# Kernel optimization log

Hardware: AMD Instinct MI355X
Metric: run time of the kernel (lower is better)

Reference implementation:

```python
import jax, jax.numpy as jnp
import numpy as np

D_MODEL = 128; D_STATE = 64; HEADDIM = 64; CHUNK = 64; EXPAND = 2
D_INNER = EXPAND * D_MODEL            # 256
NHEADS = D_INNER // HEADDIM           # 4
NGROUPS = 1; D_CONV = 4
D_XBC = D_INNER + 2 * NGROUPS * D_STATE          # 384
D_IN_PROJ = 2 * D_INNER + 2 * NGROUPS * D_STATE + NHEADS  # 644


def _segsum(x):
    # x: (..., L) -> (..., L, L) with [i, j] = sum_{j<k<=i} x_k, -inf above diag
    L = x.shape[-1]
    cs = jnp.cumsum(x, -1)
    d = cs[..., :, None] - cs[..., None, :]
    mask = jnp.tril(jnp.ones((L, L), bool))
    return jnp.where(mask, d, -jnp.inf)


def _mamba2(x, Wi, conv_w, conv_b, dt_bias, A_log, Dp, norm_w, Wo):
    b, l, _ = x.shape
    zxbcdt = x @ Wi.T                                    # (b,l,644)
    z = zxbcdt[..., :D_INNER]
    xBC = zxbcdt[..., D_INNER:D_INNER + D_XBC]
    dt = jax.nn.softplus(zxbcdt[..., D_INNER + D_XBC:] + dt_bias)  # (b,l,h)
    # causal depthwise conv1d, kernel 4
    xp = jnp.pad(xBC, ((0, 0), (D_CONV - 1, 0), (0, 0)))
    xBC = sum(xp[:, k:k + l, :] * conv_w[:, k] for k in range(D_CONV)) + conv_b
    xBC = jax.nn.silu(xBC)
    xs = xBC[..., :D_INNER].reshape(b, l, NHEADS, HEADDIM)
    Bm = xBC[..., D_INNER:D_INNER + D_STATE]             # (b,l,n) ngroups=1
    Cm = xBC[..., D_INNER + D_STATE:]                    # (b,l,n)
    A = -jnp.exp(A_log)                                  # (h,)
    # chunked SSD (ssd_minimal style)
    c = l // CHUNK
    X = xs.reshape(b, c, CHUNK, NHEADS, HEADDIM)
    dtc = dt.reshape(b, c, CHUNK, NHEADS)
    Bc = Bm.reshape(b, c, CHUNK, D_STATE)
    Cc = Cm.reshape(b, c, CHUNK, D_STATE)
    dA = jnp.transpose(dtc * A, (0, 3, 1, 2))            # (b,h,c,L)
    Acs = jnp.cumsum(dA, -1)
    Lm = jnp.exp(_segsum(dA))                            # (b,h,c,L,L)
    Xdt = X * dtc[..., None]                             # (b,c,L,h,p)
    Yd = jnp.einsum('bcln,bcsn,bhcls,bcshp->bclhp', Cc, Bc, Lm, Xdt)
    dec = jnp.exp(Acs[..., -1:] - Acs)                   # (b,h,c,L)
    st = jnp.einsum('bcln,bhcl,bclhp->bchpn', Bc, dec, Xdt)  # per-chunk states
    cd = jnp.exp(Acs[..., -1])                           # (b,h,c)
    def step(carry, inp):
        s, d = inp                                       # s:(b,h,p,n), d:(b,h)
        return carry * d[..., None, None] + s, carry
    init = jnp.zeros_like(st[:, 0])
    _, prev = jax.lax.scan(step, init, (jnp.moveaxis(st, 1, 0), jnp.moveaxis(cd, 2, 0)))
    prev = jnp.moveaxis(prev, 0, 1)                      # (b,c,h,p,n)
    Yo = jnp.einsum('bcln,bchpn,bhcl->bclhp', Cc, prev, jnp.exp(Acs))
    Y = (Yd + Yo).reshape(b, l, NHEADS, HEADDIM) + Dp[None, None, :, None] * xs
    # gated RMSNorm (norm_before_gate=False)
    y = Y.reshape(b, l, D_INNER) * jax.nn.silu(z)
    y = y * jax.lax.rsqrt(jnp.mean(y * y, -1, keepdims=True) + 1e-5) * norm_w
    return y @ Wo.T


def _init_params(key):
    ks = jax.random.split(key, 5)
    dt = jnp.exp(jax.random.uniform(ks[2], (NHEADS,)) * (np.log(0.1) - np.log(0.001)) + np.log(0.001))
    return {
        'Wi': jax.random.normal(ks[0], (D_IN_PROJ, D_MODEL), jnp.float32) * (D_MODEL ** -0.5),
        'conv_w': jax.random.normal(ks[1], (D_XBC, D_CONV), jnp.float32) * 0.3,
        'conv_b': jnp.zeros((D_XBC,), jnp.float32),
        'dt_bias': jnp.log(jnp.expm1(dt)),
        'A_log': jnp.log(jax.random.uniform(ks[3], (NHEADS,)) * 15.0 + 1.0),
        'D': jnp.ones((NHEADS,), jnp.float32),
        'norm_w': jnp.ones((D_INNER,), jnp.float32),
        'Wo': jax.random.normal(ks[4], (D_MODEL, D_INNER), jnp.float32) * (D_INNER ** -0.5),
    }


def setup_inputs() -> dict:
    key = jax.random.key(0)
    kx, kf, kb = jax.random.split(key, 3)
    inp = {'x': jax.random.normal(kx, (16, 2048, D_MODEL), jnp.float32)}
    for sfx, kk in (('_f', kf), ('_b', kb)):
        p = _init_params(kk)
        for name, v in p.items():
            inp[name + sfx] = v
    return inp


def reference(x, Wi_f, conv_w_f, conv_b_f, dt_bias_f, A_log_f, D_f, norm_w_f, Wo_f,
              Wi_b, conv_w_b, conv_b_b, dt_bias_b, A_log_b, D_b, norm_w_b, Wo_b):
    h_f = _mamba2(x, Wi_f, conv_w_f, conv_b_f, dt_bias_f, A_log_f, D_f, norm_w_f, Wo_f)
    h_b = jnp.flip(_mamba2(jnp.flip(x, 1), Wi_b, conv_w_b, conv_b_b, dt_bias_b, A_log_b, D_b, norm_w_b, Wo_b), 1)
    return h_f + h_b
```

## Files before the change

kernel.cpp:

```cpp
#include <hip/hip_runtime.h>
#include <hip/hip_bf16.h>
#include <cmath>

#define B_    16
#define L_    2048
#define T_    32768
#define DM_   128
#define DI_   256
#define DXBC_ 384
#define DS_   64
#define HD_   64
#define NH_   4
#define NC_   32

typedef __hip_bfloat16 bf16;
typedef __attribute__((ext_vector_type(8))) short short8;
typedef __attribute__((ext_vector_type(4))) float f32x4;

__device__ __forceinline__ float b2f(bf16 v) { return __bfloat162float(v); }
__device__ __forceinline__ bf16  f2b(float f) { return __float2bfloat16(f); }
__device__ __forceinline__ short f2bs(float f) { bf16 h = __float2bfloat16(f); return *reinterpret_cast<short*>(&h); }
__device__ __forceinline__ float bs2f(short s) { bf16 h = *reinterpret_cast<bf16*>(&s); return __bfloat162float(h); }
__device__ __forceinline__ float frcp_(float x) { return __builtin_amdgcn_rcpf(x); }
__device__ __forceinline__ float sigmoidf_(float x) { return frcp_(1.f + __expf(-x)); }
__device__ __forceinline__ float softplusf_(float x) { return (x > 20.f) ? x : __logf(1.f + __expf(x)); }
__device__ __forceinline__ float expneg_(float x) { return __expf(fminf(x, 0.f)); }

struct __align__(8) S4 { short a, b, c, d; };

#define NWI 82432
#define NWO 32768

__global__ __launch_bounds__(256) void k_prep(
    const float* __restrict__ x,
    const float* __restrict__ WiF, const float* __restrict__ WiB,
    const float* __restrict__ WoF, const float* __restrict__ WoB,
    bf16* __restrict__ Xb, bf16* __restrict__ WiFb, bf16* __restrict__ WiBb,
    bf16* __restrict__ WoFb, bf16* __restrict__ WoBb)
{
    const int gid = blockIdx.x * 256 + threadIdx.x;
    const int stride = gridDim.x * 256;
    for (int i = gid; i < 1048576; i += stride) {
        float4 v = ((const float4*)x)[i];
        S4 s = { f2bs(v.x), f2bs(v.y), f2bs(v.z), f2bs(v.w) };
        ((S4*)Xb)[i] = s;
    }
    for (int i = gid; i < NWI / 4; i += stride) {
        float4 v = ((const float4*)WiF)[i];
        S4 s = { f2bs(v.x), f2bs(v.y), f2bs(v.z), f2bs(v.w) };
        ((S4*)WiFb)[i] = s;
        v = ((const float4*)WiB)[i];
        S4 t = { f2bs(v.x), f2bs(v.y), f2bs(v.z), f2bs(v.w) };
        ((S4*)WiBb)[i] = t;
    }
    for (int i = gid; i < NWO / 4; i += stride) {
        float4 v = ((const float4*)WoF)[i];
        S4 s = { f2bs(v.x), f2bs(v.y), f2bs(v.z), f2bs(v.w) };
        ((S4*)WoFb)[i] = s;
        v = ((const float4*)WoB)[i];
        S4 t = { f2bs(v.x), f2bs(v.y), f2bs(v.z), f2bs(v.w) };
        ((S4*)WoBb)[i] = t;
    }
}

__global__ __launch_bounds__(256) void k_inproj_mfma(
    const bf16* __restrict__ Xb, const bf16* __restrict__ WiFb, const bf16* __restrict__ WiBb,
    const float* __restrict__ cwF, const float* __restrict__ cbF,
    const float* __restrict__ cwB, const float* __restrict__ cbB,
    const float* __restrict__ dtbF, const float* __restrict__ dtbB,
    bf16* __restrict__ Z, bf16* __restrict__ XBC, float* __restrict__ DTV)
{
    const int tid  = threadIdx.x;
    const int wave = tid >> 6, lane = tid & 63;
    const int ln15 = lane & 15, q = lane >> 4;
    const int dir  = blockIdx.y;
    const bf16* Wi = dir ? WiBb : WiFb;
    const int t0 = blockIdx.x * 64;
    const int batch = t0 >> 11, l0 = t0 & (L_ - 1);
    const size_t rowbase = (size_t)dir * T_ + t0;

    __shared__ __align__(16) short xs[80][136];
    __shared__ __align__(16) short raws[80][80];

    for (int u = tid; u < 1280; u += 256) {
        int r = u >> 4, g = u & 15;
        int l = l0 - 16 + r;
        short8 v = {0, 0, 0, 0, 0, 0, 0, 0};
        if (l >= 0) {
            int sl = dir ? (L_ - 1 - l) : l;
            v = *(const short8*)(Xb + ((size_t)batch * L_ + sl) * DM_ + g * 8);
        }
        *(short8*)&xs[r][g * 8] = v;
    }
    __syncthreads();

#pragma unroll
    for (int zt = 0; zt < 4; ++zt) {
        const int c0 = zt * 64;
        short8 wf[4];
#pragma unroll
        for (int ks = 0; ks < 4; ++ks)
            wf[ks] = *(const short8*)(Wi + (size_t)(c0 + 16 * wave + ln15) * DM_ + ks * 32 + q * 8);
#pragma unroll
        for (int ct = 0; ct < 4; ++ct) {
            f32x4 acc = (f32x4){0.f, 0.f, 0.f, 0.f};
#pragma unroll
            for (int ks = 0; ks < 4; ++ks) {
                short8 xf = *(const short8*)&xs[16 + 16 * ct + ln15][ks * 32 + q * 8];
                acc = __builtin_amdgcn_mfma_f32_16x16x32_bf16(wf[ks], xf, acc, 0, 0, 0);
            }
            S4 s = { f2bs(acc[0]), f2bs(acc[1]), f2bs(acc[2]), f2bs(acc[3]) };
            *(S4*)(Z + (rowbase + 16 * ct + ln15) * DI_ + c0 + 16 * wave + 4 * q) = s;
        }
    }

    const float* cw = dir ? cwB : cwF;
    const float* cb = dir ? cbB : cbF;
    const int c4 = (tid & 15) * 4;
    for (int nt = 4; nt < 10; ++nt) {
        const int c0 = nt * 64;
        short8 bf[4];
#pragma unroll
        for (int ks = 0; ks < 4; ++ks)
            bf[ks] = *(const short8*)(Wi + (size_t)(c0 + 16 * wave + ln15) * DM_ + ks * 32 + q * 8);
        f32x4 acc[5];
#pragma unroll
        for (int mt = 0; mt < 5; ++mt) acc[mt] = (f32x4){0.f, 0.f, 0.f, 0.f};
#pragma unroll
        for (int ks = 0; ks < 4; ++ks)
#pragma unroll
            for (int mt = 0; mt < 5; ++mt) {
                short8 afr = *(const short8*)&xs[16 * mt + ln15][ks * 32 + q * 8];
                acc[mt] = __builtin_amdgcn_mfma_f32_16x16x32_bf16(afr, bf[ks], acc[mt], 0, 0, 0);
            }
        const int ch0 = c0 - 256 + c4;
        float cwr[4][4], cbr[4];
#pragma unroll
        for (int j = 0; j < 4; ++j) {
            cbr[j] = cb[ch0 + j];
#pragma unroll
            for (int k = 0; k < 4; ++k) cwr[j][k] = cw[(ch0 + j) * 4 + k];
        }
        __syncthreads();
#pragma unroll
        for (int mt = 0; mt < 5; ++mt)
#pragma unroll
            for (int rg = 0; rg < 4; ++rg)
                raws[16 * mt + 4 * q + rg][16 * wave + ln15] = f2bs(acc[mt][rg]);
        __syncthreads();

#pragma unroll
        for (int it = 0; it < 4; ++it) {
            int row = (tid >> 4) + 16 * it;
            float s0[4];
#pragma unroll
            for (int j = 0; j < 4; ++j) s0[j] = cbr[j];
#pragma unroll
            for (int k = 0; k < 4; ++k) {
                S4 rv = *(const S4*)&raws[13 + row + k][c4];
                short rr[4] = { rv.a, rv.b, rv.c, rv.d };
#pragma unroll
                for (int j = 0; j < 4; ++j) s0[j] += bs2f(rr[j]) * cwr[j][k];
            }
            short o[4];
#pragma unroll
            for (int j = 0; j < 4; ++j) { float s = s0[j]; s = s * sigmoidf_(s); o[j] = f2bs(s); }
            S4 s4 = { o[0], o[1], o[2], o[3] };
            *(S4*)(XBC + (rowbase + row) * DXBC_ + ch0) = s4;
        }
    }

    if (wave == 0) {
        short8 bf[4];
#pragma unroll
        for (int ks = 0; ks < 4; ++ks) {
            short8 v = {0, 0, 0, 0, 0, 0, 0, 0};
            if (ln15 < 4) v = *(const short8*)(Wi + (size_t)(640 + ln15) * DM_ + ks * 32 + q * 8);
            bf[ks] = v;
        }
        const float* dtb = dir ? dtbB : dtbF;
#pragma unroll
        for (int s = 0; s < 4; ++s) {
            f32x4 acc = (f32x4){0.f, 0.f, 0.f, 0.f};
#pragma unroll
            for (int ks = 0; ks < 4; ++ks) {
                short8 afr = *(const short8*)&xs[16 + 16 * s + ln15][ks * 32 + q * 8];
                acc = __builtin_amdgcn_mfma_f32_16x16x32_bf16(afr, bf[ks], acc, 0, 0, 0);
            }
            if (ln15 < 4) {
                float bias = dtb[ln15];
#pragma unroll
                for (int rg = 0; rg < 4; ++rg)
                    DTV[(rowbase + 16 * s + 4 * q + rg) * NH_ + ln15] = softplusf_(acc[rg] + bias);
            }
        }
    }
}

__global__ __launch_bounds__(256) void k_chunkdiag_mfma(
    const bf16* __restrict__ XBC, const float* __restrict__ DTV,
    const float* __restrict__ AlF, const float* __restrict__ AlB,
    const float* __restrict__ DpF, const float* __restrict__ DpB,
    bf16* __restrict__ Y, bf16* __restrict__ ST, float* __restrict__ CDb)
{
    const int tid = threadIdx.x;
    const int wave = tid >> 6, lane = tid & 63;
    const int ln15 = lane & 15, q = lane >> 4;
    const int c = blockIdx.x;
    const int b = blockIdx.y >> 2;
    const int h = blockIdx.y & 3;
    const int dir = blockIdx.z;
    const float Ah = -__expf((dir ? AlB : AlF)[h]);
    const float Dh = (dir ? DpB : DpF)[h];
    const int t0 = b * L_ + c * 64;
    const size_t rowbase = (size_t)dir * T_ + t0;

    __shared__ __align__(16) short Bs[64][72];
    __shared__ __align__(16) short Cs[64][72];
    __shared__ __align__(16) short Xt[64][72];
    __shared__ __align__(16) short Bt[64][72];
    __shared__ float dts[64];
    __shared__ float rdts[64];
    __shared__ float Acs[64];
    __shared__ float decs[64];

    if (tid < 64) {
        int l = tid;
        float dt = DTV[(rowbase + l) * NH_ + h];
        dts[l] = dt;
        rdts[l] = frcp_(dt);
        float s = dt * Ah;
#pragma unroll
        for (int off = 1; off < 64; off <<= 1) {
            float t2 = __shfl_up(s, off);
            if (l >= off) s += t2;
        }
        Acs[l] = s;
        float alast = __shfl(s, 63);
        decs[l] = expneg_(alast - s);
        if (l == 0) CDb[(((size_t)dir * B_ + b) * NH_ + h) * NC_ + c] = expneg_(alast);
    }
    __syncthreads();

    for (int u = tid; u < 512; u += 256) {
        int r = u >> 3, g = u & 7;
        size_t base = (rowbase + r) * DXBC_;
        *(short8*)&Bs[r][g * 8] = *(const short8*)(XBC + base + 256 + g * 8);
        *(short8*)&Cs[r][g * 8] = *(const short8*)(XBC + base + 320 + g * 8);
    }
    for (int u = tid; u < 4096; u += 256) {
        int l = u >> 6, p = u & 63;
        Xt[p][l] = f2bs(b2f(XBC[(rowbase + l) * DXBC_ + h * HD_ + p]) * dts[l]);
    }
    for (int u = tid; u < 4096; u += 256) {
        int l = u >> 6, n = u & 63;
        Bt[n][l] = f2bs(b2f(XBC[(rowbase + l) * DXBC_ + 256 + n]) * decs[l]);
    }
    __syncthreads();

    f32x4 a1[4];
#pragma unroll
    for (int ct = 0; ct < 4; ++ct) a1[ct] = (f32x4){0.f, 0.f, 0.f, 0.f};
#pragma unroll
    for (int ks = 0; ks < 2; ++ks) {
        short8 afr = *(const short8*)&Cs[16 * wave + ln15][ks * 32 + q * 8];
#pragma unroll
        for (int ct = 0; ct < 4; ++ct) {
            short8 bfr = *(const short8*)&Bs[16 * ct + ln15][ks * 32 + q * 8];
            a1[ct] = __builtin_amdgcn_mfma_f32_16x16x32_bf16(afr, bfr, a1[ct], 0, 0, 0);
        }
    }
#pragma unroll
    for (int ct = 0; ct < 4; ++ct)
#pragma unroll
        for (int rg = 0; rg < 4; ++rg) {
            int l = 16 * wave + 4 * q + rg, s = 16 * ct + ln15;
            float m = (s <= l) ? a1[ct][rg] * expneg_(Acs[l] - Acs[s]) : 0.f;
            Cs[l][s] = f2bs(m);
        }
    f32x4 a2[4];
#pragma unroll
    for (int ct = 0; ct < 4; ++ct) a2[ct] = (f32x4){0.f, 0.f, 0.f, 0.f};
#pragma unroll
    for (int ks = 0; ks < 2; ++ks) {
        short8 afr = *(const short8*)&Cs[16 * wave + ln15][ks * 32 + q * 8];
#pragma unroll
        for (int ct = 0; ct < 4; ++ct) {
            short8 bfr = *(const short8*)&Xt[16 * ct + ln15][ks * 32 + q * 8];
            a2[ct] = __builtin_amdgcn_mfma_f32_16x16x32_bf16(afr, bfr, a2[ct], 0, 0, 0);
        }
    }
#pragma unroll
    for (int ct = 0; ct < 4; ++ct)
#pragma unroll
        for (int rg = 0; rg < 4; ++rg) {
            int l = 16 * wave + 4 * q + rg, p = 16 * ct + ln15;
            float xraw = bs2f(Xt[p][l]) * rdts[l];
            Y[(rowbase + l) * DI_ + h * HD_ + p] = f2b(a2[ct][rg] + Dh * xraw);
        }
    f32x4 a3[4];
#pragma unroll
    for (int ct = 0; ct < 4; ++ct) a3[ct] = (f32x4){0.f, 0.f, 0.f, 0.f};
#pragma unroll
    for (int ks = 0; ks < 2; ++ks) {
        short8 afr = *(const short8*)&Xt[16 * wave + ln15][ks * 32 + q * 8];
#pragma unroll
        for (int ct = 0; ct < 4; ++ct) {
            short8 bfr = *(const short8*)&Bt[16 * ct + ln15][ks * 32 + q * 8];
            a3[ct] = __builtin_amdgcn_mfma_f32_16x16x32_bf16(afr, bfr, a3[ct], 0, 0, 0);
        }
    }
    size_t sb = ((((size_t)dir * B_ + b) * NC_ + c) * NH_ + h) * 4096;
#pragma unroll
    for (int ct = 0; ct < 4; ++ct)
#pragma unroll
        for (int rg = 0; rg < 4; ++rg) {
            int p = 16 * wave + 4 * q + rg, n = 16 * ct + ln15;
            ST[sb + p * 64 + n] = f2b(a3[ct][rg]);
        }
}

__global__ __launch_bounds__(256) void k_scan(bf16* __restrict__ ST, const float* __restrict__ CDb)
{
    const int tid = threadIdx.x;
    const int dir = blockIdx.y;
    const int bx = blockIdx.x;
    const int b = bx >> 4, h = (bx >> 2) & 3, qt = bx & 3;
    const size_t cdbase = (((size_t)dir * B_ + b) * NH_ + h) * NC_;
    float carry[4] = {0.f, 0.f, 0.f, 0.f};
    for (int c = 0; c < NC_; ++c) {
        const float cd = CDb[cdbase + c];
        size_t base = ((((size_t)dir * B_ + b) * NC_ + c) * NH_ + h) * 4096 + qt * 1024 + tid;
#pragma unroll
        for (int q = 0; q < 4; ++q) {
            float v = b2f(ST[base + q * 256]);
            ST[base + q * 256] = f2b(carry[q]);
            carry[q] = carry[q] * cd + v;
        }
    }
}

__global__ __launch_bounds__(256) void k_offdiag_fused(
    const bf16* __restrict__ XBC, const float* __restrict__ DTV,
    const float* __restrict__ AlF, const float* __restrict__ AlB,
    const bf16* __restrict__ ST, const bf16* __restrict__ Z,
    const float* __restrict__ nwF, const float* __restrict__ nwB,
    bf16* __restrict__ Y)
{
    const int tid = threadIdx.x;
    const int wave = tid >> 6, lane = tid & 63;
    const int ln15 = lane & 15, q = lane >> 4;
    const int c = blockIdx.x, b = blockIdx.y, dir = blockIdx.z;
    const float* Al = dir ? AlB : AlF;
    const int t0 = b * L_ + c * 64;
    const size_t rowbase = (size_t)dir * T_ + t0;

    __shared__ __align__(16) short Cs[64][72];
    __shared__ __align__(16) short Ps[64][72];
    __shared__ __align__(16) short Yz[64][264];
    __shared__ float eA[NH_][64];

    {
        float A = -__expf(Al[wave]);
        float s = DTV[(rowbase + lane) * NH_ + wave] * A;
#pragma unroll
        for (int off = 1; off < 64; off <<= 1) {
            float t2 = __shfl_up(s, off);
            if (lane >= off) s += t2;
        }
        eA[wave][lane] = expneg_(s);
    }
    for (int u = tid; u < 512; u += 256) {
        int r = u >> 3, g = u & 7;
        *(short8*)&Cs[r][g * 8] = *(const short8*)(XBC + (rowbase + r) * DXBC_ + 320 + g * 8);
    }
    for (int u = lane; u < 512; u += 64) {
        int r = 16 * wave + (u >> 5), g = u & 31;
        *(short8*)&Yz[r][g * 8] = *(const short8*)(Y + (rowbase + r) * DI_ + g * 8);
    }

    for (int h = 0; h < NH_; ++h) {
        __syncthreads();
        size_t sb = ((((size_t)dir * B_ + b) * NC_ + c) * NH_ + h) * 4096;
        for (int u = tid; u < 512; u += 256) {
            int r = u >> 3, g = u & 7;
            *(short8*)&Ps[r][g * 8] = *(const short8*)(ST + sb + r * 64 + g * 8);
        }
        __syncthreads();

        f32x4 acc[4];
#pragma unroll
        for (int ct = 0; ct < 4; ++ct) acc[ct] = (f32x4){0.f, 0.f, 0.f, 0.f};
#pragma unroll
        for (int ks = 0; ks < 2; ++ks) {
            short8 afr = *(const short8*)&Cs[16 * wave + ln15][ks * 32 + q * 8];
#pragma unroll
            for (int ct = 0; ct < 4; ++ct) {
                short8 bfr = *(const short8*)&Ps[16 * ct + ln15][ks * 32 + q * 8];
                acc[ct] = __builtin_amdgcn_mfma_f32_16x16x32_bf16(afr, bfr, acc[ct], 0, 0, 0);
            }
        }
#pragma unroll
        for (int ct = 0; ct < 4; ++ct)
#pragma unroll
            for (int rg = 0; rg < 4; ++rg) {
                int l = 16 * wave + 4 * q + rg, p = 16 * ct + ln15;
                float yv = bs2f(Yz[l][h * 64 + p]) + acc[ct][rg] * eA[h][l];
                Yz[l][h * 64 + p] = f2bs(yv);
            }
    }

    const float* nw = dir ? nwB : nwF;
    float nwv[4];
#pragma unroll
    for (int j = 0; j < 4; ++j) nwv[j] = nw[lane * 4 + j];
    for (int rr = 0; rr < 16; ++rr) {
        int row = 16 * wave + rr;
        S4 zv4 = *(const S4*)(Z + (rowbase + row) * DI_ + lane * 4);
        short zr[4] = { zv4.a, zv4.b, zv4.c, zv4.d };
        float v[4]; float ss = 0.f;
#pragma unroll
        for (int j = 0; j < 4; ++j) {
            float yv = bs2f(Yz[row][lane * 4 + j]);
            float zf = bs2f(zr[j]);
            v[j] = yv * zf * sigmoidf_(zf);
            ss += v[j] * v[j];
        }
#pragma unroll
        for (int off = 1; off < 64; off <<= 1) ss += __shfl_xor(ss, off);
        float rn = rsqrtf(ss * (1.f / 256.f) + 1e-5f);
        S4 o = { f2bs(v[0] * rn * nwv[0]), f2bs(v[1] * rn * nwv[1]),
                 f2bs(v[2] * rn * nwv[2]), f2bs(v[3] * rn * nwv[3]) };
        *(S4*)(Y + (rowbase + row) * DI_ + lane * 4) = o;
    }
}

__global__ __launch_bounds__(512) void k_outproj_mfma(
    const bf16* __restrict__ Y, const bf16* __restrict__ WoFb, const bf16* __restrict__ WoBb,
    float* __restrict__ out)
{
    const int tid = threadIdx.x;
    const int wave = tid >> 6, lane = tid & 63;
    const int ln15 = lane & 15, q = lane >> 4;
    const int mt = wave & 3, nh = wave >> 2;
    const int t0 = blockIdx.x * 64;
    const int batch = t0 >> 11;
    const int l0 = t0 & (L_ - 1);

    __shared__ __align__(16) short ys[64][72];
    __shared__ __align__(16) short wsm[128][72];

    f32x4 acc[4];
#pragma unroll
    for (int ct = 0; ct < 4; ++ct) acc[ct] = (f32x4){0.f, 0.f, 0.f, 0.f};

    for (int dir = 0; dir < 2; ++dir) {
        const bf16* Wo = dir ? WoBb : WoFb;
        for (int kt = 0; kt < 4; ++kt) {
            const int k0 = kt * 64;
            __syncthreads();
            {
                int u = tid;
                int r = u >> 3, g = u & 7;
                int tsrc = dir ? (batch * L_ + (L_ - 1 - (l0 + r))) : (t0 + r);
                *(short8*)&ys[r][g * 8] =
                    *(const short8*)(Y + ((size_t)dir * T_ + tsrc) * DI_ + k0 + g * 8);
            }
            for (int u = tid; u < 1024; u += 512) {
                int m = u >> 3, g = u & 7;
                *(short8*)&wsm[m][g * 8] = *(const short8*)(Wo + (size_t)m * DI_ + k0 + g * 8);
            }
            __syncthreads();
#pragma unroll
            for (int ks = 0; ks < 2; ++ks) {
                short8 afr = *(const short8*)&ys[16 * mt + ln15][ks * 32 + q * 8];
#pragma unroll
                for (int ct = 0; ct < 4; ++ct) {
                    short8 bfr = *(const short8*)&wsm[16 * (4 * nh + ct) + ln15][ks * 32 + q * 8];
                    acc[ct] = __builtin_amdgcn_mfma_f32_16x16x32_bf16(afr, bfr, acc[ct], 0, 0, 0);
                }
            }
        }
    }
#pragma unroll
    for (int ct = 0; ct < 4; ++ct)
#pragma unroll
        for (int rg = 0; rg < 4; ++rg) {
            int row = 16 * mt + 4 * q + rg, col = 16 * (4 * nh + ct) + ln15;
            out[((size_t)(t0 + row)) * DM_ + col] = acc[ct][rg];
        }
}

extern "C" void kernel_launch(void* const* d_in, const int* in_sizes, int n_in,
                              void* d_out, int out_size, void* d_ws, size_t ws_size,
                              hipStream_t stream)
{
    const float* x    = (const float*)d_in[0];
    const float* WiF  = (const float*)d_in[1];
    const float* cwF  = (const float*)d_in[2];
    const float* cbF  = (const float*)d_in[3];
    const float* dtbF = (const float*)d_in[4];
    const float* AlF  = (const float*)d_in[5];
    const float* DpF  = (const float*)d_in[6];
    const float* nwF  = (const float*)d_in[7];
    const float* WoF  = (const float*)d_in[8];
    const float* WiB  = (const float*)d_in[9];
    const float* cwB  = (const float*)d_in[10];
    const float* cbB  = (const float*)d_in[11];
    const float* dtbB = (const float*)d_in[12];
    const float* AlB  = (const float*)d_in[13];
    const float* DpB  = (const float*)d_in[14];
    const float* nwB  = (const float*)d_in[15];
    const float* WoB  = (const float*)d_in[16];

    const size_t nZ   = (size_t)2 * T_ * DI_;
    const size_t nXBC = (size_t)2 * T_ * DXBC_;
    const size_t nY   = (size_t)2 * T_ * DI_;
    const size_t nST  = (size_t)2 * B_ * NC_ * NH_ * HD_ * DS_;
    const size_t nWb  = (size_t)2 * NWI + 2 * NWO;
    const size_t nDTV = (size_t)2 * T_ * NH_;
    const size_t nCD  = (size_t)2 * B_ * NH_ * NC_;
    const size_t need = (nZ + nXBC + nY + nST + nWb) * sizeof(bf16)
                      + (nDTV + nCD) * sizeof(float);
    if (ws_size < need) return;

    char* p = (char*)d_ws;
    bf16* Z    = (bf16*)p;            p += nZ * sizeof(bf16);
    bf16* XBC  = (bf16*)p;            p += nXBC * sizeof(bf16);
    bf16* Yb   = (bf16*)p;            p += nY * sizeof(bf16);
    bf16* ST   = (bf16*)p;            p += nST * sizeof(bf16);
    bf16* WiFb = (bf16*)p;            p += (size_t)NWI * sizeof(bf16);
    bf16* WiBb = (bf16*)p;            p += (size_t)NWI * sizeof(bf16);
    bf16* WoFb = (bf16*)p;            p += (size_t)NWO * sizeof(bf16);
    bf16* WoBb = (bf16*)p;            p += (size_t)NWO * sizeof(bf16);
    float* DTV = (float*)p;           p += nDTV * sizeof(float);
    float* CDb = (float*)p;
    bf16* Xb   = ST;

    k_prep<<<2048, 256, 0, stream>>>(x, WiF, WiB, WoF, WoB, Xb, WiFb, WiBb, WoFb, WoBb);
    k_inproj_mfma<<<dim3(512, 2), 256, 0, stream>>>(Xb, WiFb, WiBb, cwF, cbF, cwB, cbB,
                                                    dtbF, dtbB, Z, XBC, DTV);
    k_chunkdiag_mfma<<<dim3(NC_, B_ * NH_, 2), 256, 0, stream>>>(XBC, DTV, AlF, AlB, DpF, DpB,
                                                                 Yb, ST, CDb);
    k_scan<<<dim3(256, 2), 256, 0, stream>>>(ST, CDb);
    k_offdiag_fused<<<dim3(NC_, B_, 2), 256, 0, stream>>>(XBC, DTV, AlF, AlB, ST, Z,
                                                          nwF, nwB, Yb);
    k_outproj_mfma<<<dim3(512), 512, 0, stream>>>(Yb, WoFb, WoBb, (float*)d_out);
}
```

Baseline: 242.7 us.

## Fuse x bf16 conversion into inproj, share C·B^T across heads, prefetch weights/states

Drops the separate fp32→bf16 conversion pass over x and converts inside the in-projection kernel's tile load. The chunk-diagonal kernel now runs one block per (chunk, batch, dir) and loops over the 4 heads, so the C·Bᵀ product is computed once and reused; the decay scaling of B is applied on the fly in registers. The offdiag kernel keeps state tiles in registers with a one-head-ahead prefetch instead of staging them through shared memory with barriers, and the in-projection kernel prefetches the next weight tile. Fewer blocks in chunkdiag and more register pressure may lower occupancy.

```diff
diff --git a/kernel.cpp b/kernel.cpp
--- a/kernel.cpp
+++ b/kernel.cpp
@@ -21,6 +21,7 @@
 __device__ __forceinline__ bf16  f2b(float f) { return __float2bfloat16(f); }
 __device__ __forceinline__ short f2bs(float f) { bf16 h = __float2bfloat16(f); return *reinterpret_cast<short*>(&h); }
 __device__ __forceinline__ float bs2f(short s) { bf16 h = *reinterpret_cast<bf16*>(&s); return __bfloat162float(h); }
+__device__ __forceinline__ short bbits(bf16 v) { return *reinterpret_cast<short*>(&v); }
 __device__ __forceinline__ float frcp_(float x) { return __builtin_amdgcn_rcpf(x); }
 __device__ __forceinline__ float sigmoidf_(float x) { return frcp_(1.f + __expf(-x)); }
 __device__ __forceinline__ float softplusf_(float x) { return (x > 20.f) ? x : __logf(1.f + __expf(x)); }
@@ -32,19 +33,13 @@
 #define NWO 32768
 
 __global__ __launch_bounds__(256) void k_prep(
-    const float* __restrict__ x,
     const float* __restrict__ WiF, const float* __restrict__ WiB,
     const float* __restrict__ WoF, const float* __restrict__ WoB,
-    bf16* __restrict__ Xb, bf16* __restrict__ WiFb, bf16* __restrict__ WiBb,
+    bf16* __restrict__ WiFb, bf16* __restrict__ WiBb,
     bf16* __restrict__ WoFb, bf16* __restrict__ WoBb)
 {
     const int gid = blockIdx.x * 256 + threadIdx.x;
     const int stride = gridDim.x * 256;
-    for (int i = gid; i < 1048576; i += stride) {
-        float4 v = ((const float4*)x)[i];
-        S4 s = { f2bs(v.x), f2bs(v.y), f2bs(v.z), f2bs(v.w) };
-        ((S4*)Xb)[i] = s;
-    }
     for (int i = gid; i < NWI / 4; i += stride) {
         float4 v = ((const float4*)WiF)[i];
         S4 s = { f2bs(v.x), f2bs(v.y), f2bs(v.z), f2bs(v.w) };
@@ -64,7 +59,7 @@
 }
 
 __global__ __launch_bounds__(256) void k_inproj_mfma(
-    const bf16* __restrict__ Xb, const bf16* __restrict__ WiFb, const bf16* __restrict__ WiBb,
+    const float* __restrict__ x, const bf16* __restrict__ WiFb, const bf16* __restrict__ WiBb,
     const float* __restrict__ cwF, const float* __restrict__ cbF,
     const float* __restrict__ cwB, const float* __restrict__ cbB,
     const float* __restrict__ dtbF, const float* __restrict__ dtbB,
@@ -88,7 +83,11 @@
         short8 v = {0, 0, 0, 0, 0, 0, 0, 0};
         if (l >= 0) {
             int sl = dir ? (L_ - 1 - l) : l;
-            v = *(const short8*)(Xb + ((size_t)batch * L_ + sl) * DM_ + g * 8);
+            const float* xp = x + ((size_t)batch * L_ + sl) * DM_ + g * 8;
+            float4 a = *(const float4*)xp;
+            float4 bb = *(const float4*)(xp + 4);
+            v = (short8){ f2bs(a.x), f2bs(a.y), f2bs(a.z), f2bs(a.w),
+                          f2bs(bb.x), f2bs(bb.y), f2bs(bb.z), f2bs(bb.w) };
         }
         *(short8*)&xs[r][g * 8] = v;
     }
@@ -117,12 +116,12 @@
     const float* cw = dir ? cwB : cwF;
     const float* cb = dir ? cbB : cbF;
     const int c4 = (tid & 15) * 4;
+    short8 bcur[4];
+#pragma unroll
+    for (int ks = 0; ks < 4; ++ks)
+        bcur[ks] = *(const short8*)(Wi + (size_t)(256 + 16 * wave + ln15) * DM_ + ks * 32 + q * 8);
     for (int nt = 4; nt < 10; ++nt) {
         const int c0 = nt * 64;
-        short8 bf[4];
-#pragma unroll
-        for (int ks = 0; ks < 4; ++ks)
-            bf[ks] = *(const short8*)(Wi + (size_t)(c0 + 16 * wave + ln15) * DM_ + ks * 32 + q * 8);
         f32x4 acc[5];
 #pragma unroll
         for (int mt = 0; mt < 5; ++mt) acc[mt] = (f32x4){0.f, 0.f, 0.f, 0.f};
@@ -131,8 +130,14 @@
 #pragma unroll
             for (int mt = 0; mt < 5; ++mt) {
                 short8 afr = *(const short8*)&xs[16 * mt + ln15][ks * 32 + q * 8];
-                acc[mt] = __builtin_amdgcn_mfma_f32_16x16x32_bf16(afr, bf[ks], acc[mt], 0, 0, 0);
-            }
+                acc[mt] = __builtin_amdgcn_mfma_f32_16x16x32_bf16(afr, bcur[ks], acc[mt], 0, 0, 0);
+            }
+        short8 bnxt[4];
+        if (nt < 9) {
+#pragma unroll
+            for (int ks = 0; ks < 4; ++ks)
+                bnxt[ks] = *(const short8*)(Wi + (size_t)(c0 + 64 + 16 * wave + ln15) * DM_ + ks * 32 + q * 8);
+        }
         const int ch0 = c0 - 256 + c4;
         float cwr[4][4], cbr[4];
 #pragma unroll
@@ -168,15 +173,17 @@
             S4 s4 = { o[0], o[1], o[2], o[3] };
             *(S4*)(XBC + (rowbase + row) * DXBC_ + ch0) = s4;
         }
+#pragma unroll
+        for (int ks = 0; ks < 4; ++ks) bcur[ks] = bnxt[ks];
     }
 
     if (wave == 0) {
-        short8 bf[4];
+        short8 bfr[4];
 #pragma unroll
         for (int ks = 0; ks < 4; ++ks) {
             short8 v = {0, 0, 0, 0, 0, 0, 0, 0};
             if (ln15 < 4) v = *(const short8*)(Wi + (size_t)(640 + ln15) * DM_ + ks * 32 + q * 8);
-            bf[ks] = v;
+            bfr[ks] = v;
         }
         const float* dtb = dir ? dtbB : dtbF;
 #pragma unroll
@@ -185,7 +192,7 @@
 #pragma unroll
             for (int ks = 0; ks < 4; ++ks) {
                 short8 afr = *(const short8*)&xs[16 + 16 * s + ln15][ks * 32 + q * 8];
-                acc = __builtin_amdgcn_mfma_f32_16x16x32_bf16(afr, bf[ks], acc, 0, 0, 0);
+                acc = __builtin_amdgcn_mfma_f32_16x16x32_bf16(afr, bfr[ks], acc, 0, 0, 0);
             }
             if (ln15 < 4) {
                 float bias = dtb[ln15];
@@ -206,42 +213,35 @@
     const int tid = threadIdx.x;
     const int wave = tid >> 6, lane = tid & 63;
     const int ln15 = lane & 15, q = lane >> 4;
-    const int c = blockIdx.x;
-    const int b = blockIdx.y >> 2;
-    const int h = blockIdx.y & 3;
-    const int dir = blockIdx.z;
-    const float Ah = -__expf((dir ? AlB : AlF)[h]);
-    const float Dh = (dir ? DpB : DpF)[h];
+    const int c = blockIdx.x, b = blockIdx.y, dir = blockIdx.z;
+    const float* Al = dir ? AlB : AlF;
+    const float* Dp = dir ? DpB : DpF;
     const int t0 = b * L_ + c * 64;
     const size_t rowbase = (size_t)dir * T_ + t0;
 
     __shared__ __align__(16) short Bs[64][72];
     __shared__ __align__(16) short Cs[64][72];
+    __shared__ __align__(16) short Ms[64][72];
+    __shared__ __align__(16) short Bt[64][72];
     __shared__ __align__(16) short Xt[64][72];
-    __shared__ __align__(16) short Bt[64][72];
-    __shared__ float dts[64];
-    __shared__ float rdts[64];
-    __shared__ float Acs[64];
-    __shared__ float decs[64];
-
-    if (tid < 64) {
-        int l = tid;
-        float dt = DTV[(rowbase + l) * NH_ + h];
-        dts[l] = dt;
-        rdts[l] = frcp_(dt);
+    __shared__ float dtsS[NH_][64], AcsS[NH_][64], decS[NH_][64], rdtS[NH_][64];
+
+    {
+        float Ah = -__expf(Al[wave]);
+        float dt = DTV[(rowbase + lane) * NH_ + wave];
+        dtsS[wave][lane] = dt;
+        rdtS[wave][lane] = frcp_(dt);
         float s = dt * Ah;
 #pragma unroll
         for (int off = 1; off < 64; off <<= 1) {
             float t2 = __shfl_up(s, off);
-            if (l >= off) s += t2;
-        }
-        Acs[l] = s;
+            if (lane >= off) s += t2;
+        }
+        AcsS[wave][lane] = s;
         float alast = __shfl(s, 63);
-        decs[l] = expneg_(alast - s);
-        if (l == 0) CDb[(((size_t)dir * B_ + b) * NH_ + h) * NC_ + c] = expneg_(alast);
-    }
-    __syncthreads();
-
+        decS[wave][lane] = expneg_(alast - s);
+        if (lane == 0) CDb[(((size_t)dir * B_ + b) * NH_ + wave) * NC_ + c] = expneg_(alast);
+    }
     for (int u = tid; u < 512; u += 256) {
         int r = u >> 3, g = u & 7;
         size_t base = (rowbase + r) * DXBC_;
@@ -249,75 +249,88 @@
         *(short8*)&Cs[r][g * 8] = *(const short8*)(XBC + base + 320 + g * 8);
     }
     for (int u = tid; u < 4096; u += 256) {
-        int l = u >> 6, p = u & 63;
-        Xt[p][l] = f2bs(b2f(XBC[(rowbase + l) * DXBC_ + h * HD_ + p]) * dts[l]);
-    }
-    for (int u = tid; u < 4096; u += 256) {
         int l = u >> 6, n = u & 63;
-        Bt[n][l] = f2bs(b2f(XBC[(rowbase + l) * DXBC_ + 256 + n]) * decs[l]);
+        Bt[n][l] = bbits(XBC[(rowbase + l) * DXBC_ + 256 + n]);
     }
     __syncthreads();
 
-    f32x4 a1[4];
-#pragma unroll
-    for (int ct = 0; ct < 4; ++ct) a1[ct] = (f32x4){0.f, 0.f, 0.f, 0.f};
+    f32x4 g4[4];
+#pragma unroll
+    for (int ct = 0; ct < 4; ++ct) g4[ct] = (f32x4){0.f, 0.f, 0.f, 0.f};
 #pragma unroll
     for (int ks = 0; ks < 2; ++ks) {
         short8 afr = *(const short8*)&Cs[16 * wave + ln15][ks * 32 + q * 8];
 #pragma unroll
         for (int ct = 0; ct < 4; ++ct) {
             short8 bfr = *(const short8*)&Bs[16 * ct + ln15][ks * 32 + q * 8];
-            a1[ct] = __builtin_amdgcn_mfma_f32_16x16x32_bf16(afr, bfr, a1[ct], 0, 0, 0);
-        }
-    }
-#pragma unroll
-    for (int ct = 0; ct < 4; ++ct)
-#pragma unroll
-        for (int rg = 0; rg < 4; ++rg) {
-            int l = 16 * wave + 4 * q + rg, s = 16 * ct + ln15;
-            float m = (s <= l) ? a1[ct][rg] * expneg_(Acs[l] - Acs[s]) : 0.f;
-            Cs[l][s] = f2bs(m);
-        }
-    f32x4 a2[4];
-#pragma unroll
-    for (int ct = 0; ct < 4; ++ct) a2[ct] = (f32x4){0.f, 0.f, 0.f, 0.f};
-#pragma unroll
-    for (int ks = 0; ks < 2; ++ks) {
-        short8 afr = *(const short8*)&Cs[16 * wave + ln15][ks * 32 + q * 8];
-#pragma unroll
-        for (int ct = 0; ct < 4; ++ct) {
-            short8 bfr = *(const short8*)&Xt[16 * ct + ln15][ks * 32 + q * 8];
-            a2[ct] = __builtin_amdgcn_mfma_f32_16x16x32_bf16(afr, bfr, a2[ct], 0, 0, 0);
-        }
-    }
-#pragma unroll
-    for (int ct = 0; ct < 4; ++ct)
-#pragma unroll
-        for (int rg = 0; rg < 4; ++rg) {
-            int l = 16 * wave + 4 * q + rg, p = 16 * ct + ln15;
-            float xraw = bs2f(Xt[p][l]) * rdts[l];
-            Y[(rowbase + l) * DI_ + h * HD_ + p] = f2b(a2[ct][rg] + Dh * xraw);
-        }
-    f32x4 a3[4];
-#pragma unroll
-    for (int ct = 0; ct < 4; ++ct) a3[ct] = (f32x4){0.f, 0.f, 0.f, 0.f};
-#pragma unroll
-    for (int ks = 0; ks < 2; ++ks) {
-        short8 afr = *(const short8*)&Xt[16 * wave + ln15][ks * 32 + q * 8];
-#pragma unroll
-        for (int ct = 0; ct < 4; ++ct) {
-            short8 bfr = *(const short8*)&Bt[16 * ct + ln15][ks * 32 + q * 8];
-            a3[ct] = __builtin_amdgcn_mfma_f32_16x16x32_bf16(afr, bfr, a3[ct], 0, 0, 0);
-        }
-    }
-    size_t sb = ((((size_t)dir * B_ + b) * NC_ + c) * NH_ + h) * 4096;
-#pragma unroll
-    for (int ct = 0; ct < 4; ++ct)
-#pragma unroll
-        for (int rg = 0; rg < 4; ++rg) {
-            int p = 16 * wave + 4 * q + rg, n = 16 * ct + ln15;
-            ST[sb + p * 64 + n] = f2b(a3[ct][rg]);
-        }
+            g4[ct] = __builtin_amdgcn_mfma_f32_16x16x32_bf16(afr, bfr, g4[ct], 0, 0, 0);
+        }
+    }
+
+    for (int h = 0; h < NH_; ++h) {
+        if (h > 0) __syncthreads();
+        for (int u = tid; u < 4096; u += 256) {
+            int l = u >> 6, p = u & 63;
+            Xt[p][l] = f2bs(b2f(XBC[(rowbase + l) * DXBC_ + h * HD_ + p]) * dtsS[h][l]);
+        }
+        __syncthreads();
+
+#pragma unroll
+        for (int ct = 0; ct < 4; ++ct)
+#pragma unroll
+            for (int rg = 0; rg < 4; ++rg) {
+                int l = 16 * wave + 4 * q + rg, s = 16 * ct + ln15;
+                float m = (s <= l) ? g4[ct][rg] * expneg_(AcsS[h][l] - AcsS[h][s]) : 0.f;
+                Ms[l][s] = f2bs(m);
+            }
+        f32x4 a2[4];
+#pragma unroll
+        for (int ct = 0; ct < 4; ++ct) a2[ct] = (f32x4){0.f, 0.f, 0.f, 0.f};
+#pragma unroll
+        for (int ks = 0; ks < 2; ++ks) {
+            short8 afr = *(const short8*)&Ms[16 * wave + ln15][ks * 32 + q * 8];
+#pragma unroll
+            for (int ct = 0; ct < 4; ++ct) {
+                short8 bfr = *(const short8*)&Xt[16 * ct + ln15][ks * 32 + q * 8];
+                a2[ct] = __builtin_amdgcn_mfma_f32_16x16x32_bf16(afr, bfr, a2[ct], 0, 0, 0);
+            }
+        }
+        const float Dh = Dp[h];
+#pragma unroll
+        for (int ct = 0; ct < 4; ++ct)
+#pragma unroll
+            for (int rg = 0; rg < 4; ++rg) {
+                int l = 16 * wave + 4 * q + rg, p = 16 * ct + ln15;
+                float xraw = bs2f(Xt[p][l]) * rdtS[h][l];
+                Y[(rowbase + l) * DI_ + h * HD_ + p] = f2b(a2[ct][rg] + Dh * xraw);
+            }
+        f32x4 a3[4];
+#pragma unroll
+        for (int ct = 0; ct < 4; ++ct) a3[ct] = (f32x4){0.f, 0.f, 0.f, 0.f};
+#pragma unroll
+        for (int ks = 0; ks < 2; ++ks) {
+            short8 afr = *(const short8*)&Xt[16 * wave + ln15][ks * 32 + q * 8];
+            float dk[8];
+#pragma unroll
+            for (int j = 0; j < 8; ++j) dk[j] = decS[h][ks * 32 + q * 8 + j];
+#pragma unroll
+            for (int ct = 0; ct < 4; ++ct) {
+                short8 raw = *(const short8*)&Bt[16 * ct + ln15][ks * 32 + q * 8];
+                short8 bfr;
+#pragma unroll
+                for (int j = 0; j < 8; ++j) bfr[j] = f2bs(bs2f(raw[j]) * dk[j]);
+                a3[ct] = __builtin_amdgcn_mfma_f32_16x16x32_bf16(afr, bfr, a3[ct], 0, 0, 0);
+            }
+        }
+        size_t sb = ((((size_t)dir * B_ + b) * NC_ + c) * NH_ + h) * 4096;
+#pragma unroll
+        for (int ct = 0; ct < 4; ++ct)
+#pragma unroll
+            for (int rg = 0; rg < 4; ++rg) {
+                int p = 16 * wave + 4 * q + rg, n = 16 * ct + ln15;
+                ST[sb + p * 64 + n] = f2b(a3[ct][rg]);
+            }
+    }
 }
 
 __global__ __launch_bounds__(256) void k_scan(bf16* __restrict__ ST, const float* __restrict__ CDb)
@@ -354,11 +367,18 @@
     const float* Al = dir ? AlB : AlF;
     const int t0 = b * L_ + c * 64;
     const size_t rowbase = (size_t)dir * T_ + t0;
+    const size_t sbase = ((((size_t)dir * B_ + b) * NC_ + c) * NH_) * 4096;
 
     __shared__ __align__(16) short Cs[64][72];
-    __shared__ __align__(16) short Ps[64][72];
     __shared__ __align__(16) short Yz[64][264];
     __shared__ float eA[NH_][64];
+
+    short8 pcur[4][2], pnxt[4][2];
+#pragma unroll
+    for (int ct = 0; ct < 4; ++ct)
+#pragma unroll
+        for (int ks = 0; ks < 2; ++ks)
+            pcur[ct][ks] = *(const short8*)(ST + sbase + (16 * ct + ln15) * 64 + ks * 32 + q * 8);
 
     {
         float A = -__expf(Al[wave]);
@@ -378,28 +398,31 @@
         int r = 16 * wave + (u >> 5), g = u & 31;
         *(short8*)&Yz[r][g * 8] = *(const short8*)(Y + (rowbase + r) * DI_ + g * 8);
     }
-
+    __syncthreads();
+
+    short8 cfr[2];
+#pragma unroll
+    for (int ks = 0; ks < 2; ++ks)
+        cfr[ks] = *(const short8*)&Cs[16 * wave + ln15][ks * 32 + q * 8];
+
+#pragma unroll
     for (int h = 0; h < NH_; ++h) {
-        __syncthreads();
-        size_t sb = ((((size_t)dir * B_ + b) * NC_ + c) * NH_ + h) * 4096;
-        for (int u = tid; u < 512; u += 256) {
-            int r = u >> 3, g = u & 7;
-            *(short8*)&Ps[r][g * 8] = *(const short8*)(ST + sb + r * 64 + g * 8);
-        }
-        __syncthreads();
-
+        if (h < 3) {
+#pragma unroll
+            for (int ct = 0; ct < 4; ++ct)
+#pragma unroll
+                for (int ks = 0; ks < 2; ++ks)
+                    pnxt[ct][ks] = *(const short8*)(ST + sbase + (size_t)(h + 1) * 4096
+                                                    + (16 * ct + ln15) * 64 + ks * 32 + q * 8);
+        }
         f32x4 acc[4];
 #pragma unroll
         for (int ct = 0; ct < 4; ++ct) acc[ct] = (f32x4){0.f, 0.f, 0.f, 0.f};
 #pragma unroll
-        for (int ks = 0; ks < 2; ++ks) {
-            short8 afr = *(const short8*)&Cs[16 * wave + ln15][ks * 32 + q * 8];
-#pragma unroll
-            for (int ct = 0; ct < 4; ++ct) {
-                short8 bfr = *(const short8*)&Ps[16 * ct + ln15][ks * 32 + q * 8];
-                acc[ct] = __builtin_amdgcn_mfma_f32_16x16x32_bf16(afr, bfr, acc[ct], 0, 0, 0);
-            }
-        }
+        for (int ks = 0; ks < 2; ++ks)
+#pragma unroll
+            for (int ct = 0; ct < 4; ++ct)
+                acc[ct] = __builtin_amdgcn_mfma_f32_16x16x32_bf16(cfr[ks], pcur[ct][ks], acc[ct], 0, 0, 0);
 #pragma unroll
         for (int ct = 0; ct < 4; ++ct)
 #pragma unroll
@@ -408,6 +431,11 @@
                 float yv = bs2f(Yz[l][h * 64 + p]) + acc[ct][rg] * eA[h][l];
                 Yz[l][h * 64 + p] = f2bs(yv);
             }
+#pragma unroll
+        for (int ct = 0; ct < 4; ++ct)
+#pragma unroll
+            for (int ks = 0; ks < 2; ++ks)
+                pcur[ct][ks] = pnxt[ct][ks];
     }
 
     const float* nw = dir ? nwB : nwF;
@@ -535,13 +563,12 @@
     bf16* WoBb = (bf16*)p;            p += (size_t)NWO * sizeof(bf16);
     float* DTV = (float*)p;           p += nDTV * sizeof(float);
     float* CDb = (float*)p;
-    bf16* Xb   = ST;
-
-    k_prep<<<2048, 256, 0, stream>>>(x, WiF, WiB, WoF, WoB, Xb, WiFb, WiBb, WoFb, WoBb);
-    k_inproj_mfma<<<dim3(512, 2), 256, 0, stream>>>(Xb, WiFb, WiBb, cwF, cbF, cwB, cbB,
+
+    k_prep<<<128, 256, 0, stream>>>(WiF, WiB, WoF, WoB, WiFb, WiBb, WoFb, WoBb);
+    k_inproj_mfma<<<dim3(512, 2), 256, 0, stream>>>(x, WiFb, WiBb, cwF, cbF, cwB, cbB,
                                                     dtbF, dtbB, Z, XBC, DTV);
-    k_chunkdiag_mfma<<<dim3(NC_, B_ * NH_, 2), 256, 0, stream>>>(XBC, DTV, AlF, AlB, DpF, DpB,
-                                                                 Yb, ST, CDb);
+    k_chunkdiag_mfma<<<dim3(NC_, B_, 2), 256, 0, stream>>>(XBC, DTV, AlF, AlB, DpF, DpB,
+                                                           Yb, ST, CDb);
     k_scan<<<dim3(256, 2), 256, 0, stream>>>(ST, CDb);
     k_offdiag_fused<<<dim3(NC_, B_, 2), 256, 0, stream>>>(XBC, DTV, AlF, AlB, ST, Z,
                                                           nwF, nwB, Yb);
```

Measured after the change: 251.9 us. 1.04x slower.
